# Optimization experiments

Hardware: AMD Instinct MI355X
Metric: run time of the kernel (lower is better)

## Reference

```python
import jax, jax.numpy as jnp
import numpy as np

N_CELLS_RNA, N_GENES = 8000, 8000
N_CELLS_ATAC, N_REGIONS = 8000, 20000
N_FACTORS = 100

def setup_inputs() -> dict:
    key = jax.random.key(0)
    ks = jax.random.split(key, 10)
    return {
        "G": jax.random.uniform(ks[0], (N_CELLS_RNA, N_GENES), jnp.float32),
        "R": jax.random.uniform(ks[1], (N_CELLS_ATAC, N_REGIONS), jnp.float32),
        "A": jax.random.uniform(ks[2], (N_GENES, N_REGIONS), jnp.float32),
        "C_1": jax.random.uniform(ks[3], (N_CELLS_RNA, N_FACTORS), jnp.float32),
        "C_2": jax.random.uniform(ks[4], (N_CELLS_ATAC, N_FACTORS), jnp.float32),
        "C_g": jax.random.uniform(ks[5], (N_GENES, N_FACTORS), jnp.float32),
        "C_r": jax.random.uniform(ks[6], (N_REGIONS, N_FACTORS), jnp.float32),
        "A_g": jax.random.normal(ks[7], (N_FACTORS, N_FACTORS), jnp.float32),
        "A_r": jax.random.normal(ks[8], (N_FACTORS, N_FACTORS), jnp.float32),
        "b_g": jnp.zeros((1, N_GENES), jnp.float32),
        "b_r": jnp.zeros((1, N_REGIONS), jnp.float32),
        "b_1": jnp.zeros((N_CELLS_RNA, 1), jnp.float32),
        "b_2": jnp.zeros((N_CELLS_ATAC, 1), jnp.float32),
        "alpha": jnp.array([1000.0, 1000.0, 100.0, 10.0, 0.0], jnp.float32),
    }

def reference(G, R, A, C_1, C_2, C_g, C_r, A_g, A_r, b_g, b_r, b_1, b_2, alpha):
    sm = lambda X: jax.nn.softmax(X, axis=1)  # row-wise softmax as in torch dim=1
    S1, S2, Sg, Sr = sm(C_1), sm(C_2), sm(C_g), sm(C_r)
    # loss1: RNA reconstruction. [n1,N]@[N,N] then @[N,ng]
    rec_G = (S1 @ A_g) @ Sg.T
    loss1 = jnp.mean(jnp.square(G - rec_G - b_g - b_1))
    # loss2: ATAC reconstruction
    rec_R = (S2 @ A_r) @ Sr.T
    loss2 = jnp.mean(jnp.square(R - rec_R - b_r - b_2))
    # loss3: -trace(A_r^T A_g) / ||A_r|| / ||A_g||
    loss3 = -jnp.sum(A_r * A_g) / jnp.linalg.norm(A_r) / jnp.linalg.norm(A_g)
    # loss4: -trace(Sg^T (A Sr)) / ||Sg|| / ||A Sr||  (trace via elementwise sum)
    ASr = A @ Sr  # [ng, N]
    loss4 = -jnp.sum(Sg * ASr) / jnp.linalg.norm(Sg) / jnp.linalg.norm(ASr)
    l1 = alpha[0] * loss1
    l2 = alpha[1] * loss2
    l3 = alpha[2] * loss3
    l4 = alpha[3] * loss4
    loss = l1 + l2 + l3 + l4
    return jnp.stack([loss, l1, l2, l3, l4])
```

## Files before the change

kernel.cpp:

```cpp
#include <hip/hip_runtime.h>
#include <hip/hip_bf16.h>

typedef __bf16 bf16x8 __attribute__((ext_vector_type(8)));
typedef float  f32x4  __attribute__((ext_vector_type(4)));
typedef unsigned short us4 __attribute__((ext_vector_type(4)));

#define N_CELLS 8000
#define N_GENES 8000
#define N_REG   20000
#define NF      100
#define KP      128
#define NFT     112
#define KSPLIT  25

static __device__ __forceinline__ unsigned short f2bf_bits(float f) {
  unsigned u = __builtin_bit_cast(unsigned, f);
  u = (u + 0x7FFFu + ((u >> 16) & 1u)) >> 16;
  return (unsigned short)u;
}
static __device__ __forceinline__ float bf2f(unsigned short s) {
  unsigned u = ((unsigned)s) << 16;
  return __builtin_bit_cast(float, u);
}
static __device__ __forceinline__ bf16x8 cvt8n(f32x4 v0, f32x4 v1) {
  bf16x8 r;
  r[0] = __builtin_bit_cast(__bf16, __float2bfloat16(v0[0]));
  r[1] = __builtin_bit_cast(__bf16, __float2bfloat16(v0[1]));
  r[2] = __builtin_bit_cast(__bf16, __float2bfloat16(v0[2]));
  r[3] = __builtin_bit_cast(__bf16, __float2bfloat16(v0[3]));
  r[4] = __builtin_bit_cast(__bf16, __float2bfloat16(v1[0]));
  r[5] = __builtin_bit_cast(__bf16, __float2bfloat16(v1[1]));
  r[6] = __builtin_bit_cast(__bf16, __float2bfloat16(v1[2]));
  r[7] = __builtin_bit_cast(__bf16, __float2bfloat16(v1[3]));
  return r;
}

__global__ __launch_bounds__(64) void pre_kernel(
    const float* __restrict__ C1, const float* __restrict__ C2,
    const float* __restrict__ Cg, const float* __restrict__ Cr,
    const float* __restrict__ Ag, const float* __restrict__ Ar,
    unsigned short* __restrict__ T1, unsigned short* __restrict__ T2,
    unsigned short* __restrict__ Sg, unsigned short* __restrict__ Sr,
    unsigned short* __restrict__ SrT,
    float* __restrict__ accv) {
  __shared__ float srow[NF];
  int b = blockIdx.x, t = threadIdx.x;
  if (b >= 44000) {
    float d = 0.f, na = 0.f, nr = 0.f;
    for (int i = t; i < NF * NF; i += 64) {
      float a = Ag[i], r = Ar[i];
      d = fmaf(a, r, d); na = fmaf(a, a, na); nr = fmaf(r, r, nr);
    }
    #pragma unroll
    for (int off = 32; off > 0; off >>= 1) {
      d += __shfl_xor(d, off); na += __shfl_xor(na, off); nr += __shfl_xor(nr, off);
    }
    if (t == 0) { accv[2] = d; accv[3] = na; accv[4] = nr; }
    return;
  }
  const float* C; const float* W = nullptr;
  unsigned short* outR = nullptr; unsigned short* outT = nullptr;
  bool isSr = false;
  int i;
  if (b < 8000)       { C = C1; W = Ag; outT = T1; i = b; }
  else if (b < 16000) { C = C2; W = Ar; outT = T2; i = b - 8000; }
  else if (b < 24000) { C = Cg; outR = Sg; i = b - 16000; }
  else                { C = Cr; outR = Sr; isSr = true; i = b - 24000; }

  float v0 = C[i * NF + t];
  float v1 = (t < 36) ? C[i * NF + 64 + t] : -3.0e38f;
  float m = fmaxf(v0, v1);
  #pragma unroll
  for (int off = 32; off > 0; off >>= 1) m = fmaxf(m, __shfl_xor(m, off));
  float e0 = __expf(v0 - m);
  float e1 = (t < 36) ? __expf(v1 - m) : 0.f;
  float s = e0 + e1;
  #pragma unroll
  for (int off = 32; off > 0; off >>= 1) s += __shfl_xor(s, off);
  float inv = 1.f / s;
  e0 *= inv; e1 *= inv;

  if (outT == nullptr) {
    unsigned short b0 = f2bf_bits(e0);
    unsigned short b1 = (t < 36) ? f2bf_bits(e1) : (unsigned short)0;
    outR[i * KP + t] = b0;
    outR[i * KP + 64 + t] = b1;
    if (isSr) {
      SrT[t * N_REG + i] = b0;
      if (t < 48) SrT[(64 + t) * N_REG + i] = b1;
    }
    return;
  }
  srow[t] = e0;
  if (t < 36) srow[64 + t] = e1;
  __syncthreads();
  int c2 = 64 + t;
  int c2c = (c2 < NF) ? c2 : NF - 1;
  float a0=0.f, a1=0.f, a2=0.f, a3=0.f;
  float d0=0.f, d1=0.f, d2=0.f, d3=0.f;
  #pragma unroll 4
  for (int k = 0; k < NF; k += 4) {
    float s0 = srow[k], s1 = srow[k+1], s2 = srow[k+2], s3 = srow[k+3];
    a0 = fmaf(s0, W[(k  )*NF + t], a0);
    a1 = fmaf(s1, W[(k+1)*NF + t], a1);
    a2 = fmaf(s2, W[(k+2)*NF + t], a2);
    a3 = fmaf(s3, W[(k+3)*NF + t], a3);
    d0 = fmaf(s0, W[(k  )*NF + c2c], d0);
    d1 = fmaf(s1, W[(k+1)*NF + c2c], d1);
    d2 = fmaf(s2, W[(k+2)*NF + c2c], d2);
    d3 = fmaf(s3, W[(k+3)*NF + c2c], d3);
  }
  outT[i * KP + t]  = f2bf_bits((a0 + a1) + (a2 + a3));
  outT[i * KP + c2] = (c2 < NF) ? f2bf_bits((d0 + d1) + (d2 + d3)) : (unsigned short)0;
}

__global__ __launch_bounds__(256, 3) void resid_kernel(
    const float* __restrict__ X,
    const unsigned short* __restrict__ Tm,
    const unsigned short* __restrict__ Sm,
    const float* __restrict__ bcol,
    const float* __restrict__ brow,
    int N, float* __restrict__ buckets) {
  __shared__ char ldsbuf[49152];
  char* ldsT = ldsbuf;
  char* ldsS = ldsbuf + 16384;
  int t = threadIdx.x;
  int wid = t >> 6, lane = t & 63;
  int lr = lane & 15, lg = lane >> 4;
  long r0blk = (long)blockIdx.y * 64;
  long c0blk = (long)blockIdx.x * 128;
  int r0 = (wid >> 1) * 32;
  int c0 = (wid & 1) * 64;

  bf16x8 sT[4], sS[8];
  #pragma unroll
  for (int i2 = 0; i2 < 4; ++i2) {
    int g = i2 * 256 + t, row = g >> 4, gi = g & 15;
    sT[i2] = *reinterpret_cast<const bf16x8*>(Tm + (r0blk + row) * KP + gi * 8);
  }
  #pragma unroll
  for (int i2 = 0; i2 < 8; ++i2) {
    int g = i2 * 256 + t, row = g >> 4, gi = g & 15;
    sS[i2] = *reinterpret_cast<const bf16x8*>(Sm + (c0blk + row) * KP + gi * 8);
  }

  f32x4 xv[2][4];
  #pragma unroll
  for (int ri = 0; ri < 2; ++ri) {
    long row = r0blk + r0 + ri * 16 + lr;
    #pragma unroll
    for (int ci = 0; ci < 4; ++ci) {
      long cb = c0blk + c0 + ci * 16 + lg * 4;
      if (cb < N) xv[ri][ci] = *reinterpret_cast<const f32x4*>(X + row * N + cb);
      else        xv[ri][ci] = f32x4{0.f, 0.f, 0.f, 0.f};
    }
  }

  #pragma unroll
  for (int i2 = 0; i2 < 4; ++i2) {
    int g = i2 * 256 + t, row = g >> 4, gi = g & 15;
    int off = row * 256 + ((gi * 16) ^ ((row & 7) << 4));
    *reinterpret_cast<bf16x8*>(ldsT + off) = sT[i2];
  }
  #pragma unroll
  for (int i2 = 0; i2 < 8; ++i2) {
    int g = i2 * 256 + t, row = g >> 4, gi = g & 15;
    int off = row * 256 + ((gi * 16) ^ ((row & 7) << 4));
    *reinterpret_cast<bf16x8*>(ldsS + off) = sS[i2];
  }
  __syncthreads();

  f32x4 zero = {0.f, 0.f, 0.f, 0.f};
  f32x4 acc[4][2] = {{zero, zero}, {zero, zero}, {zero, zero}, {zero, zero}};
  #pragma unroll
  for (int ks = 0; ks < 4; ++ks) {
    bf16x8 a[4], bfr[2];
    #pragma unroll
    for (int ci = 0; ci < 4; ++ci) {
      int row = c0 + ci * 16 + lr;
      int off = row * 256 + (((ks * 64) + (lg * 16)) ^ ((row & 7) << 4));
      a[ci] = *reinterpret_cast<const bf16x8*>(ldsS + off);
    }
    #pragma unroll
    for (int ri = 0; ri < 2; ++ri) {
      int row = r0 + ri * 16 + lr;
      int off = row * 256 + (((ks * 64) + (lg * 16)) ^ ((row & 7) << 4));
      bfr[ri] = *reinterpret_cast<const bf16x8*>(ldsT + off);
    }
    #pragma unroll
    for (int ci = 0; ci < 4; ++ci)
      #pragma unroll
      for (int ri = 0; ri < 2; ++ri)
        acc[ci][ri] = __builtin_amdgcn_mfma_f32_16x16x32_bf16(a[ci], bfr[ri], acc[ci][ri], 0, 0, 0);
  }

  float brv[2];
  #pragma unroll
  for (int ri = 0; ri < 2; ++ri) brv[ri] = brow[r0blk + r0 + ri * 16 + lr];

  float sse = 0.f;
  #pragma unroll
  for (int ci = 0; ci < 4; ++ci) {
    long cb = c0blk + c0 + ci * 16 + lg * 4;
    if (cb < N) {
      f32x4 bc = *reinterpret_cast<const f32x4*>(bcol + cb);
      #pragma unroll
      for (int ri = 0; ri < 2; ++ri) {
        f32x4 x = xv[ri][ci];
        #pragma unroll
        for (int j = 0; j < 4; ++j) {
          float e = x[j] - acc[ci][ri][j] - bc[j] - brv[ri];
          sse = fmaf(e, e, sse);
        }
      }
    }
  }
  #pragma unroll
  for (int off = 32; off > 0; off >>= 1) sse += __shfl_xor(sse, off);
  __shared__ float wsum[4];
  if (lane == 0) wsum[wid] = sse;
  __syncthreads();
  if (t == 0)
    atomicAdd(&buckets[(blockIdx.y * gridDim.x + blockIdx.x) & 63],
              wsum[0] + wsum[1] + wsum[2] + wsum[3]);
}

__global__ __launch_bounds__(256, 4) void asr_kernel(
    const float* __restrict__ A,
    const unsigned short* __restrict__ SrT,
    float* __restrict__ ASrN) {
  __shared__ char lds[2][16384];
  int t = threadIdx.x;
  int w = t >> 6, lane = t & 63;
  int lr = lane & 15, lg = lane >> 4;
  int gBase = blockIdx.x * 64;
  int kb0 = blockIdx.y * 800;

  const unsigned short* pb = SrT + (long)lr * N_REG + lg * 8;

  f32x4 zero = {0.f, 0.f, 0.f, 0.f};
  f32x4 acc[7] = {zero, zero, zero, zero, zero, zero, zero};
  f32x4 sreg[8];

  #pragma unroll
  for (int p = 0; p < 4; ++p) {
    int flat = p * 2048 + t * 8;
    int row = flat >> 7, kk = flat & 127;
    const float* src = A + (long)(gBase + row) * N_REG + kb0 + kk;
    sreg[2 * p]     = *reinterpret_cast<const f32x4*>(src);
    sreg[2 * p + 1] = *reinterpret_cast<const f32x4*>(src + 4);
  }

  #pragma unroll 1
  for (int it = 0; it < 7; ++it) {
    char* buf = lds[it & 1];
    if (it < 6) {
      #pragma unroll
      for (int p = 0; p < 4; ++p) {
        int flat = p * 2048 + t * 8;
        int row = flat >> 7, kk = flat & 127;
        int off = row * 256 + ((kk * 2) ^ ((row & 7) << 4));
        *reinterpret_cast<bf16x8*>(buf + off) = cvt8n(sreg[2 * p], sreg[2 * p + 1]);
      }
    } else {
      int row = t >> 2, kk = (t & 3) * 8;
      int off = row * 256 + ((kk * 2) ^ ((row & 7) << 4));
      *reinterpret_cast<bf16x8*>(buf + off) = cvt8n(sreg[0], sreg[1]);
    }
    __syncthreads();

    if (it < 5) {
      #pragma unroll
      for (int p = 0; p < 4; ++p) {
        int flat = p * 2048 + t * 8;
        int row = flat >> 7, kk = flat & 127;
        const float* src = A + (long)(gBase + row) * N_REG + kb0 + (it + 1) * 128 + kk;
        sreg[2 * p]     = *reinterpret_cast<const f32x4*>(src);
        sreg[2 * p + 1] = *reinterpret_cast<const f32x4*>(src + 4);
      }
    } else if (it == 5) {
      int row = t >> 2, kk = (t & 3) * 8;
      const float* src = A + (long)(gBase + row) * N_REG + kb0 + 768 + kk;
      sreg[0] = *reinterpret_cast<const f32x4*>(src);
      sreg[1] = *reinterpret_cast<const f32x4*>(src + 4);
    }

    int kb = kb0 + it * 128;
    int arow = w * 16 + lr;
    int nk = (it < 6) ? 4 : 1;
    #pragma unroll 4
    for (int ks = 0; ks < nk; ++ks) {
      int off = arow * 256 + (((ks * 64) + lg * 16) ^ ((arow & 7) << 4));
      bf16x8 ag = *reinterpret_cast<const bf16x8*>(buf + off);
      #pragma unroll
      for (int ni = 0; ni < 7; ++ni) {
        bf16x8 b = *reinterpret_cast<const bf16x8*>(pb + (long)ni * 16 * N_REG + kb + ks * 32);
        acc[ni] = __builtin_amdgcn_mfma_f32_16x16x32_bf16(ag, b, acc[ni], 0, 0, 0);
      }
    }
  }

  float* slice = ASrN + (long)blockIdx.y * (N_GENES * NFT);
  int g0 = gBase + w * 16;
  #pragma unroll
  for (int ni = 0; ni < 7; ++ni) {
    int f = ni * 16 + lr;
    #pragma unroll
    for (int j = 0; j < 4; ++j)
      slice[(g0 + lg * 4 + j) * NFT + f] = acc[ni][j];
  }
}

__global__ void l4red_kernel(const unsigned short* __restrict__ Sgbf,
                             const float* __restrict__ ASrN,
                             float* __restrict__ accv) {
  const int NV = N_GENES * NFT / 4;
  int t = blockIdx.x * blockDim.x + threadIdx.x;
  float d = 0.f, n1 = 0.f, n2 = 0.f;
  for (int q = t; q < NV; q += gridDim.x * blockDim.x) {
    int g = q / (NFT / 4);
    int f4 = (q - g * (NFT / 4)) * 4;
    f32x4 av = {0.f, 0.f, 0.f, 0.f};
    #pragma unroll
    for (int s = 0; s < KSPLIT; ++s)
      av += *reinterpret_cast<const f32x4*>(ASrN + (long)s * (N_GENES * NFT) + g * NFT + f4);
    us4 sgb = *reinterpret_cast<const us4*>(Sgbf + g * KP + f4);
    #pragma unroll
    for (int j = 0; j < 4; ++j) {
      float sg = bf2f(sgb[j]);
      d = fmaf(sg, av[j], d); n1 = fmaf(sg, sg, n1); n2 = fmaf(av[j], av[j], n2);
    }
  }
  #pragma unroll
  for (int off = 32; off > 0; off >>= 1) {
    d += __shfl_xor(d, off); n1 += __shfl_xor(n1, off); n2 += __shfl_xor(n2, off);
  }
  __shared__ float r3[3][4];
  int lane = threadIdx.x & 63, w = threadIdx.x >> 6;
  if (lane == 0) { r3[0][w] = d; r3[1][w] = n1; r3[2][w] = n2; }
  __syncthreads();
  if (threadIdx.x == 0) {
    atomicAdd(&accv[5], r3[0][0] + r3[0][1] + r3[0][2] + r3[0][3]);
    atomicAdd(&accv[6], r3[1][0] + r3[1][1] + r3[1][2] + r3[1][3]);
    atomicAdd(&accv[7], r3[2][0] + r3[2][1] + r3[2][2] + r3[2][3]);
  }
}

__global__ void fin_kernel(const float* __restrict__ accv,
                           const float* __restrict__ bk1,
                           const float* __restrict__ bk2,
                           const float* __restrict__ alpha,
                           float* __restrict__ out) {
  if (threadIdx.x == 0) {
    float s1 = 0.f, s2 = 0.f;
    for (int i = 0; i < 64; ++i) { s1 += bk1[i]; s2 += bk2[i]; }
    float loss1 = s1 / 64000000.0f;
    float loss2 = s2 / 160000000.0f;
    float loss3 = -accv[2] / (sqrtf(accv[3]) * sqrtf(accv[4]));
    float loss4 = -accv[5] / (sqrtf(accv[6]) * sqrtf(accv[7]));
    float l1 = alpha[0] * loss1, l2 = alpha[1] * loss2;
    float l3 = alpha[2] * loss3, l4 = alpha[3] * loss4;
    out[0] = l1 + l2 + l3 + l4;
    out[1] = l1; out[2] = l2; out[3] = l3; out[4] = l4;
  }
}


extern "C" void kernel_launch(void* const* d_in, const int* in_sizes, int n_in,
                              void* d_out, int out_size, void* d_ws, size_t ws_size,
                              hipStream_t stream) {
  const float* G  = (const float*)d_in[0];
  const float* R  = (const float*)d_in[1];
  const float* A  = (const float*)d_in[2];
  const float* C1 = (const float*)d_in[3];
  const float* C2 = (const float*)d_in[4];
  const float* Cg = (const float*)d_in[5];
  const float* Cr = (const float*)d_in[6];
  const float* Ag = (const float*)d_in[7];
  const float* Ar = (const float*)d_in[8];
  const float* bg = (const float*)d_in[9];
  const float* br = (const float*)d_in[10];
  const float* b1 = (const float*)d_in[11];
  const float* b2 = (const float*)d_in[12];
  const float* alpha = (const float*)d_in[13];

  char* ws = (char*)d_ws;
  float* accv           = (float*)(ws + 0);
  float* buckets1       = (float*)(ws + 64);
  float* buckets2       = (float*)(ws + 320);
  float* ASrN           = (float*)(ws + 1024);
  unsigned short* T1    = (unsigned short*)(ws + 89601024);
  unsigned short* T2    = (unsigned short*)(ws + 91649024);
  unsigned short* Sg    = (unsigned short*)(ws + 93697024);
  unsigned short* Sr    = (unsigned short*)(ws + 95745024);
  unsigned short* SrT   = (unsigned short*)(ws + 100865024);

  hipMemsetAsync(d_ws, 0, 576, stream);

  pre_kernel<<<44001, 64, 0, stream>>>(C1, C2, Cg, Cr, Ag, Ar,
                                       T1, T2, Sg, Sr, SrT, accv);

  resid_kernel<<<dim3(63, 125), 256, 0, stream>>>(G, T1, Sg, bg, b1, N_GENES, buckets1);
  resid_kernel<<<dim3(157, 125), 256, 0, stream>>>(R, T2, Sr, br, b2, N_REG, buckets2);

  asr_kernel<<<dim3(125, KSPLIT), 256, 0, stream>>>(A, SrT, ASrN);

  l4red_kernel<<<128, 256, 0, stream>>>(Sg, ASrN, accv);
  fin_kernel<<<1, 64, 0, stream>>>(accv, buckets1, buckets2, alpha, (float*)d_out);
}
```

Measured before the change: 650.5 us.

## Pack four softmax rows per block, add LDS transpose kernel, use nontemporal loads

After: 645.1 us. About the same (-0.8%).

```diff
diff --git a/kernel.cpp b/kernel.cpp
--- a/kernel.cpp
+++ b/kernel.cpp
@@ -4,6 +4,7 @@
 typedef __bf16 bf16x8 __attribute__((ext_vector_type(8)));
 typedef float  f32x4  __attribute__((ext_vector_type(4)));
 typedef unsigned short us4 __attribute__((ext_vector_type(4)));
+typedef unsigned short us8 __attribute__((ext_vector_type(8)));
 
 #define N_CELLS 8000
 #define N_GENES 8000
@@ -35,19 +36,19 @@
   return r;
 }
 
-__global__ __launch_bounds__(64) void pre_kernel(
+__global__ __launch_bounds__(256) void pre_kernel(
     const float* __restrict__ C1, const float* __restrict__ C2,
     const float* __restrict__ Cg, const float* __restrict__ Cr,
     const float* __restrict__ Ag, const float* __restrict__ Ar,
     unsigned short* __restrict__ T1, unsigned short* __restrict__ T2,
     unsigned short* __restrict__ Sg, unsigned short* __restrict__ Sr,
-    unsigned short* __restrict__ SrT,
     float* __restrict__ accv) {
-  __shared__ float srow[NF];
+  __shared__ float srow[4][NF];
   int b = blockIdx.x, t = threadIdx.x;
-  if (b >= 44000) {
+  int w = t >> 6, lane = t & 63;
+  if (b == 11000) {
     float d = 0.f, na = 0.f, nr = 0.f;
-    for (int i = t; i < NF * NF; i += 64) {
+    for (int i = t; i < NF * NF; i += 256) {
       float a = Ag[i], r = Ar[i];
       d = fmaf(a, r, d); na = fmaf(a, a, na); nr = fmaf(r, r, nr);
     }
@@ -55,25 +56,31 @@
     for (int off = 32; off > 0; off >>= 1) {
       d += __shfl_xor(d, off); na += __shfl_xor(na, off); nr += __shfl_xor(nr, off);
     }
-    if (t == 0) { accv[2] = d; accv[3] = na; accv[4] = nr; }
+    __shared__ float r3[3][4];
+    if (lane == 0) { r3[0][w] = d; r3[1][w] = na; r3[2][w] = nr; }
+    __syncthreads();
+    if (t == 0) {
+      accv[2] = r3[0][0] + r3[0][1] + r3[0][2] + r3[0][3];
+      accv[3] = r3[1][0] + r3[1][1] + r3[1][2] + r3[1][3];
+      accv[4] = r3[2][0] + r3[2][1] + r3[2][2] + r3[2][3];
+    }
     return;
   }
   const float* C; const float* W = nullptr;
   unsigned short* outR = nullptr; unsigned short* outT = nullptr;
-  bool isSr = false;
   int i;
-  if (b < 8000)       { C = C1; W = Ag; outT = T1; i = b; }
-  else if (b < 16000) { C = C2; W = Ar; outT = T2; i = b - 8000; }
-  else if (b < 24000) { C = Cg; outR = Sg; i = b - 16000; }
-  else                { C = Cr; outR = Sr; isSr = true; i = b - 24000; }
-
-  float v0 = C[i * NF + t];
-  float v1 = (t < 36) ? C[i * NF + 64 + t] : -3.0e38f;
+  if (b < 2000)      { C = C1; W = Ag; outT = T1; i = b * 4 + w; }
+  else if (b < 4000) { C = C2; W = Ar; outT = T2; i = (b - 2000) * 4 + w; }
+  else if (b < 6000) { C = Cg; outR = Sg; i = (b - 4000) * 4 + w; }
+  else               { C = Cr; outR = Sr; i = (b - 6000) * 4 + w; }
+
+  float v0 = C[i * NF + lane];
+  float v1 = (lane < 36) ? C[i * NF + 64 + lane] : -3.0e38f;
   float m = fmaxf(v0, v1);
   #pragma unroll
   for (int off = 32; off > 0; off >>= 1) m = fmaxf(m, __shfl_xor(m, off));
   float e0 = __expf(v0 - m);
-  float e1 = (t < 36) ? __expf(v1 - m) : 0.f;
+  float e1 = (lane < 36) ? __expf(v1 - m) : 0.f;
   float s = e0 + e1;
   #pragma unroll
   for (int off = 32; off > 0; off >>= 1) s += __shfl_xor(s, off);
@@ -81,37 +88,61 @@
   e0 *= inv; e1 *= inv;
 
   if (outT == nullptr) {
-    unsigned short b0 = f2bf_bits(e0);
-    unsigned short b1 = (t < 36) ? f2bf_bits(e1) : (unsigned short)0;
-    outR[i * KP + t] = b0;
-    outR[i * KP + 64 + t] = b1;
-    if (isSr) {
-      SrT[t * N_REG + i] = b0;
-      if (t < 48) SrT[(64 + t) * N_REG + i] = b1;
-    }
+    outR[i * KP + lane] = f2bf_bits(e0);
+    outR[i * KP + 64 + lane] = (lane < 36) ? f2bf_bits(e1) : (unsigned short)0;
     return;
   }
-  srow[t] = e0;
-  if (t < 36) srow[64 + t] = e1;
+  srow[w][lane] = e0;
+  if (lane < 36) srow[w][64 + lane] = e1;
   __syncthreads();
-  int c2 = 64 + t;
+  int c2 = 64 + lane;
   int c2c = (c2 < NF) ? c2 : NF - 1;
   float a0=0.f, a1=0.f, a2=0.f, a3=0.f;
   float d0=0.f, d1=0.f, d2=0.f, d3=0.f;
   #pragma unroll 4
   for (int k = 0; k < NF; k += 4) {
-    float s0 = srow[k], s1 = srow[k+1], s2 = srow[k+2], s3 = srow[k+3];
-    a0 = fmaf(s0, W[(k  )*NF + t], a0);
-    a1 = fmaf(s1, W[(k+1)*NF + t], a1);
-    a2 = fmaf(s2, W[(k+2)*NF + t], a2);
-    a3 = fmaf(s3, W[(k+3)*NF + t], a3);
+    float s0 = srow[w][k], s1 = srow[w][k+1], s2 = srow[w][k+2], s3 = srow[w][k+3];
+    a0 = fmaf(s0, W[(k  )*NF + lane], a0);
+    a1 = fmaf(s1, W[(k+1)*NF + lane], a1);
+    a2 = fmaf(s2, W[(k+2)*NF + lane], a2);
+    a3 = fmaf(s3, W[(k+3)*NF + lane], a3);
     d0 = fmaf(s0, W[(k  )*NF + c2c], d0);
     d1 = fmaf(s1, W[(k+1)*NF + c2c], d1);
     d2 = fmaf(s2, W[(k+2)*NF + c2c], d2);
     d3 = fmaf(s3, W[(k+3)*NF + c2c], d3);
   }
-  outT[i * KP + t]  = f2bf_bits((a0 + a1) + (a2 + a3));
-  outT[i * KP + c2] = (c2 < NF) ? f2bf_bits((d0 + d1) + (d2 + d3)) : (unsigned short)0;
+  outT[i * KP + lane] = f2bf_bits((a0 + a1) + (a2 + a3));
+  outT[i * KP + c2]   = (c2 < NF) ? f2bf_bits((d0 + d1) + (d2 + d3)) : (unsigned short)0;
+}
+
+__global__ __launch_bounds__(256) void trT_kernel(
+    const unsigned short* __restrict__ Sr,
+    unsigned short* __restrict__ SrT) {
+  __shared__ unsigned short lds[64 * 128];
+  int t = threadIdx.x;
+  long r0 = (long)blockIdx.x * 64;
+  int nv = (int)((N_REG - r0 < 64) ? (N_REG - r0) : 64);
+  #pragma unroll
+  for (int q = 0; q < 4; ++q) {
+    int idx = q * 256 + t;
+    int row = idx >> 4, col8 = (idx & 15) * 8;
+    us8 v = {0, 0, 0, 0, 0, 0, 0, 0};
+    if (row < nv) v = *reinterpret_cast<const us8*>(Sr + (r0 + row) * KP + col8);
+    *reinterpret_cast<us8*>(lds + row * 128 + col8) = v;
+  }
+  __syncthreads();
+  if (t < NFT) {
+    int f = t;
+    #pragma unroll
+    for (int c = 0; c < 8; ++c) {
+      if (c * 8 < nv) {
+        us8 v;
+        #pragma unroll
+        for (int j = 0; j < 8; ++j) v[j] = lds[(c * 8 + j) * 128 + f];
+        *reinterpret_cast<us8*>(SrT + (long)f * N_REG + r0 + c * 8) = v;
+      }
+    }
+  }
 }
 
 __global__ __launch_bounds__(256, 3) void resid_kernel(
@@ -151,7 +182,8 @@
     #pragma unroll
     for (int ci = 0; ci < 4; ++ci) {
       long cb = c0blk + c0 + ci * 16 + lg * 4;
-      if (cb < N) xv[ri][ci] = *reinterpret_cast<const f32x4*>(X + row * N + cb);
+      if (cb < N) xv[ri][ci] = __builtin_nontemporal_load(
+                    reinterpret_cast<const f32x4*>(X + row * N + cb));
       else        xv[ri][ci] = f32x4{0.f, 0.f, 0.f, 0.f};
     }
   }
@@ -247,8 +279,8 @@
     int flat = p * 2048 + t * 8;
     int row = flat >> 7, kk = flat & 127;
     const float* src = A + (long)(gBase + row) * N_REG + kb0 + kk;
-    sreg[2 * p]     = *reinterpret_cast<const f32x4*>(src);
-    sreg[2 * p + 1] = *reinterpret_cast<const f32x4*>(src + 4);
+    sreg[2 * p]     = __builtin_nontemporal_load(reinterpret_cast<const f32x4*>(src));
+    sreg[2 * p + 1] = __builtin_nontemporal_load(reinterpret_cast<const f32x4*>(src + 4));
   }
 
   #pragma unroll 1
@@ -275,14 +307,14 @@
         int flat = p * 2048 + t * 8;
         int row = flat >> 7, kk = flat & 127;
         const float* src = A + (long)(gBase + row) * N_REG + kb0 + (it + 1) * 128 + kk;
-        sreg[2 * p]     = *reinterpret_cast<const f32x4*>(src);
-        sreg[2 * p + 1] = *reinterpret_cast<const f32x4*>(src + 4);
+        sreg[2 * p]     = __builtin_nontemporal_load(reinterpret_cast<const f32x4*>(src));
+        sreg[2 * p + 1] = __builtin_nontemporal_load(reinterpret_cast<const f32x4*>(src + 4));
       }
     } else if (it == 5) {
       int row = t >> 2, kk = (t & 3) * 8;
       const float* src = A + (long)(gBase + row) * N_REG + kb0 + 768 + kk;
-      sreg[0] = *reinterpret_cast<const f32x4*>(src);
-      sreg[1] = *reinterpret_cast<const f32x4*>(src + 4);
+      sreg[0] = __builtin_nontemporal_load(reinterpret_cast<const f32x4*>(src));
+      sreg[1] = __builtin_nontemporal_load(reinterpret_cast<const f32x4*>(src + 4));
     }
 
     int kb = kb0 + it * 128;
@@ -307,7 +339,7 @@
     int f = ni * 16 + lr;
     #pragma unroll
     for (int j = 0; j < 4; ++j)
-      slice[(g0 + lg * 4 + j) * NFT + f] = acc[ni][j];
+      __builtin_nontemporal_store(acc[ni][j], &slice[(g0 + lg * 4 + j) * NFT + f]);
   }
 }
 
@@ -323,7 +355,8 @@
     f32x4 av = {0.f, 0.f, 0.f, 0.f};
     #pragma unroll
     for (int s = 0; s < KSPLIT; ++s)
-      av += *reinterpret_cast<const f32x4*>(ASrN + (long)s * (N_GENES * NFT) + g * NFT + f4);
+      av += __builtin_nontemporal_load(
+              reinterpret_cast<const f32x4*>(ASrN + (long)s * (N_GENES * NFT) + g * NFT + f4));
     us4 sgb = *reinterpret_cast<const us4*>(Sgbf + g * KP + f4);
     #pragma unroll
     for (int j = 0; j < 4; ++j) {
@@ -397,8 +430,9 @@
 
   hipMemsetAsync(d_ws, 0, 576, stream);
 
-  pre_kernel<<<44001, 64, 0, stream>>>(C1, C2, Cg, Cr, Ag, Ar,
-                                       T1, T2, Sg, Sr, SrT, accv);
+  pre_kernel<<<11001, 256, 0, stream>>>(C1, C2, Cg, Cr, Ag, Ar,
+                                        T1, T2, Sg, Sr, accv);
+  trT_kernel<<<313, 256, 0, stream>>>(Sr, SrT);
 
   resid_kernel<<<dim3(63, 125), 256, 0, stream>>>(G, T1, Sg, bg, b1, N_GENES, buckets1);
   resid_kernel<<<dim3(157, 125), 256, 0, stream>>>(R, T2, Sr, br, b2, N_REG, buckets2);
```
